# Optimization experiments

Measured on AMD Instinct MI355X. Metric: run time of the kernel, lower is better.

## Reference

```python
import jax, jax.numpy as jnp
import numpy as np

N_NODES = 100000
N_EDGES = 1000000
H = 128


def setup_inputs() -> dict:
    key = jax.random.key(0)
    ks = jax.random.split(key, 8)
    s = 1.0 / np.sqrt(H)
    return {
        "x": jax.random.normal(ks[0], (N_NODES, H), dtype=jnp.float32),
        "edge_index": jax.random.randint(ks[1], (2, N_EDGES), 0, N_NODES, dtype=jnp.int64),
        "W_p": jax.random.normal(ks[2], (H, H), dtype=jnp.float32) * s,
        "b_p": jnp.zeros((H,), dtype=jnp.float32),
        "W_c": jax.random.normal(ks[3], (H, H), dtype=jnp.float32) * s,
        "b_c": jnp.zeros((H,), dtype=jnp.float32),
        "W1": jax.random.normal(ks[4], (3 * H, H), dtype=jnp.float32) * (1.0 / np.sqrt(3 * H)),
        "b1": jnp.zeros((H,), dtype=jnp.float32),
        "W2": jax.random.normal(ks[5], (H, 1), dtype=jnp.float32) * s,
        "b2": jnp.zeros((1,), dtype=jnp.float32),
    }


def reference(x, edge_index, W_p, b_p, W_c, b_c, W1, b1, W2, b2):
    # Gather parent (src) and child (dst) node features per edge: [E, H]
    par_fea = x[edge_index[0]]
    cld_fea = x[edge_index[1]]
    # Dual small MLPs (LeakyReLU slope 0.01, dropout inactive at inference)
    enc_p = jax.nn.leaky_relu(par_fea @ W_p + b_p, negative_slope=0.01)
    enc_c = jax.nn.leaky_relu(cld_fea @ W_c + b_c, negative_slope=0.01)
    diff = jnp.abs(par_fea - cld_fea)
    edge_features = jnp.concatenate([enc_p, enc_c, diff], axis=-1)  # [E, 3H]
    h = jax.nn.relu(edge_features @ W1 + b1)
    edge_weight = jax.nn.sigmoid(h @ W2 + b2).squeeze(-1)  # [E]
    return edge_weight
```

## Files before the change

kernel.cpp:

```cpp
#include <hip/hip_runtime.h>
#include <hip/hip_bf16.h>

#define E_EDGES 1000000
#define N_NODES 100000
#define HDIM 128
#define BM 64
#define LDP 136

typedef __attribute__((ext_vector_type(8))) short short8;
typedef __attribute__((ext_vector_type(4))) float f32x4;

static __device__ __forceinline__ short f2bf(float f) {
  unsigned int u = __float_as_uint(f);
  unsigned int r = (u + 0x7FFFu + ((u >> 16) & 1u)) >> 16;
  return (short)r;
}
static __device__ __forceinline__ float bf2f(short s) {
  return __uint_as_float(((unsigned int)(unsigned short)s) << 16);
}

__global__ void prep_weights(const float* __restrict__ Wp, const float* __restrict__ Wc,
                             const float* __restrict__ W1, const float* __restrict__ W2,
                             short* __restrict__ wp_t, short* __restrict__ wc_t,
                             short* __restrict__ w1_t, float* __restrict__ w2v) {
  int i = blockIdx.x * 256 + threadIdx.x;
  if (i < HDIM * HDIM) {
    int o = i >> 7, k = i & (HDIM - 1);
    wp_t[i] = f2bf(Wp[k * HDIM + o]);
    wc_t[i] = f2bf(Wc[k * HDIM + o]);
  }
  if (i < HDIM * 3 * HDIM) {
    int o = i / (3 * HDIM), k = i - o * (3 * HDIM);
    w1_t[i] = f2bf(W1[k * HDIM + o]);
  }
  if (i < HDIM) w2v[i] = W2[i];
}

__global__ __launch_bounds__(256) void node_precompute(
    const float* __restrict__ x, const float* __restrict__ b_p,
    const float* __restrict__ b_c, const float* __restrict__ b1,
    const short* __restrict__ wp_t, const short* __restrict__ wc_t,
    const short* __restrict__ w1_t,
    short* __restrict__ x_bf, short* __restrict__ Abuf, short* __restrict__ Bbuf) {
  __shared__ __align__(16) short Xt[BM * LDP];
  __shared__ __align__(16) short Yp[BM * LDP];
  __shared__ __align__(16) short Yc[BM * LDP];

  const int t = threadIdx.x;
  const int n0 = blockIdx.x * BM;

  {
    const int lane16 = t & 15, rq = t >> 4, c0 = lane16 * 8;
#pragma unroll
    for (int pass = 0; pass < 4; ++pass) {
      const int row = pass * 16 + rq;
      const int n = n0 + row;
      short8 v;
      if (n < N_NODES) {
        const float* ps = x + (size_t)n * HDIM + c0;
        float4 a = *(const float4*)ps;
        float4 b = *(const float4*)(ps + 4);
        float f[8] = {a.x, a.y, a.z, a.w, b.x, b.y, b.z, b.w};
#pragma unroll
        for (int j = 0; j < 8; ++j) v[j] = f2bf(f[j]);
        *(short8*)&x_bf[(size_t)n * HDIM + c0] = v;
      } else {
#pragma unroll
        for (int j = 0; j < 8; ++j) v[j] = 0;
      }
      *(short8*)&Xt[row * LDP + c0] = v;
    }
  }
  __syncthreads();

  const int l = t & 63;
  const int w = t >> 6;
  const int lr = l & 15;
  const int lg = l >> 4;
  const int aoff = lr * LDP + lg * 8;
  const int na = w * 32 + lr, nb = na + 16;

  const f32x4 zero4 = {0.f, 0.f, 0.f, 0.f};
  f32x4 ap_[4][2], ac_[4][2];
#pragma unroll
  for (int mi = 0; mi < 4; ++mi) {
    ap_[mi][0] = zero4; ap_[mi][1] = zero4;
    ac_[mi][0] = zero4; ac_[mi][1] = zero4;
  }

  const short* wpA = wp_t + na * HDIM + lg * 8;
  const short* wpB = wp_t + nb * HDIM + lg * 8;
  const short* wcA = wc_t + na * HDIM + lg * 8;
  const short* wcB = wc_t + nb * HDIM + lg * 8;

#pragma unroll
  for (int kk = 0; kk < 4; ++kk) {
    short8 b10 = *(const short8*)(wpA + kk * 32);
    short8 b11 = *(const short8*)(wpB + kk * 32);
    short8 b20 = *(const short8*)(wcA + kk * 32);
    short8 b21 = *(const short8*)(wcB + kk * 32);
#pragma unroll
    for (int mi = 0; mi < 4; ++mi) {
      short8 a8 = *(const short8*)&Xt[mi * 16 * LDP + aoff + kk * 32];
      ap_[mi][0] = __builtin_amdgcn_mfma_f32_16x16x32_bf16(a8, b10, ap_[mi][0], 0, 0, 0);
      ap_[mi][1] = __builtin_amdgcn_mfma_f32_16x16x32_bf16(a8, b11, ap_[mi][1], 0, 0, 0);
      ac_[mi][0] = __builtin_amdgcn_mfma_f32_16x16x32_bf16(a8, b20, ac_[mi][0], 0, 0, 0);
      ac_[mi][1] = __builtin_amdgcn_mfma_f32_16x16x32_bf16(a8, b21, ac_[mi][1], 0, 0, 0);
    }
  }

  {
    const float bpa = b_p[na], bpb = b_p[nb];
    const float bca = b_c[na], bcb = b_c[nb];
#pragma unroll
    for (int mi = 0; mi < 4; ++mi) {
#pragma unroll
      for (int r = 0; r < 4; ++r) {
        const int m = mi * 16 + lg * 4 + r;
        float v0 = ap_[mi][0][r] + bpa; v0 = v0 > 0.f ? v0 : 0.01f * v0;
        float v1 = ap_[mi][1][r] + bpb; v1 = v1 > 0.f ? v1 : 0.01f * v1;
        float u0 = ac_[mi][0][r] + bca; u0 = u0 > 0.f ? u0 : 0.01f * u0;
        float u1 = ac_[mi][1][r] + bcb; u1 = u1 > 0.f ? u1 : 0.01f * u1;
        Yp[m * LDP + na] = f2bf(v0);
        Yp[m * LDP + nb] = f2bf(v1);
        Yc[m * LDP + na] = f2bf(u0);
        Yc[m * LDP + nb] = f2bf(u1);
      }
    }
  }
  __syncthreads();

  f32x4 aa_[4][2], ab_[4][2];
#pragma unroll
  for (int mi = 0; mi < 4; ++mi) {
    aa_[mi][0] = zero4; aa_[mi][1] = zero4;
    ab_[mi][0] = zero4; ab_[mi][1] = zero4;
  }
  const short* w1Aa = w1_t + na * (3 * HDIM) + lg * 8;
  const short* w1Ab = w1_t + nb * (3 * HDIM) + lg * 8;
#pragma unroll
  for (int kk = 0; kk < 4; ++kk) {
    short8 ba0 = *(const short8*)(w1Aa + kk * 32);
    short8 ba1 = *(const short8*)(w1Ab + kk * 32);
    short8 bb0 = *(const short8*)(w1Aa + HDIM + kk * 32);
    short8 bb1 = *(const short8*)(w1Ab + HDIM + kk * 32);
#pragma unroll
    for (int mi = 0; mi < 4; ++mi) {
      short8 ayp = *(const short8*)&Yp[mi * 16 * LDP + aoff + kk * 32];
      short8 ayc = *(const short8*)&Yc[mi * 16 * LDP + aoff + kk * 32];
      aa_[mi][0] = __builtin_amdgcn_mfma_f32_16x16x32_bf16(ayp, ba0, aa_[mi][0], 0, 0, 0);
      aa_[mi][1] = __builtin_amdgcn_mfma_f32_16x16x32_bf16(ayp, ba1, aa_[mi][1], 0, 0, 0);
      ab_[mi][0] = __builtin_amdgcn_mfma_f32_16x16x32_bf16(ayc, bb0, ab_[mi][0], 0, 0, 0);
      ab_[mi][1] = __builtin_amdgcn_mfma_f32_16x16x32_bf16(ayc, bb1, ab_[mi][1], 0, 0, 0);
    }
  }

  {
    const float b1a = b1[na], b1b = b1[nb];
#pragma unroll
    for (int mi = 0; mi < 4; ++mi) {
#pragma unroll
      for (int r = 0; r < 4; ++r) {
        const int m = mi * 16 + lg * 4 + r;
        const int n = n0 + m;
        if (n < N_NODES) {
          Abuf[(size_t)n * HDIM + na] = f2bf(aa_[mi][0][r] + b1a);
          Abuf[(size_t)n * HDIM + nb] = f2bf(aa_[mi][1][r] + b1b);
          Bbuf[(size_t)n * HDIM + na] = f2bf(ab_[mi][0][r]);
          Bbuf[(size_t)n * HDIM + nb] = f2bf(ab_[mi][1][r]);
        }
      }
    }
  }
}

__global__ __launch_bounds__(512, 8) void edge_kernel(
    const int* __restrict__ ei, const short* __restrict__ x_bf,
    const short* __restrict__ Abuf, const short* __restrict__ Bbuf,
    const short* __restrict__ w1_t, const float* __restrict__ w2v,
    const float* __restrict__ b2, float* __restrict__ out) {
  __shared__ __align__(16) short Dt[BM * LDP];
  __shared__ float partial[8][BM];

  const int t = threadIdx.x;
  const int e0 = blockIdx.x * BM;

  {
    const int lane16 = t & 15, rq = t >> 4, c0 = lane16 * 8;
#pragma unroll
    for (int pass = 0; pass < 2; ++pass) {
      const int row = pass * 32 + rq;
      const int s = ei[e0 + row];
      const int d = ei[E_EDGES + e0 + row];
      short8 p8 = *(const short8*)(x_bf + (size_t)s * HDIM + c0);
      short8 c8 = *(const short8*)(x_bf + (size_t)d * HDIM + c0);
      short8 v;
#pragma unroll
      for (int j = 0; j < 8; ++j) v[j] = f2bf(fabsf(bf2f(p8[j]) - bf2f(c8[j])));
      *(short8*)&Dt[row * LDP + c0] = v;
    }
  }

  const int l = t & 63;
  const int w = t >> 6;
  const int lr = l & 15;
  const int lg = l >> 4;
  const int na = w * 16 + lr;
  const int aoff = lr * LDP + lg * 8;

  f32x4 acc[4];
#pragma unroll
  for (int mi = 0; mi < 4; ++mi) {
#pragma unroll
    for (int r = 0; r < 4; ++r) {
      const int m = mi * 16 + lg * 4 + r;
      const int s = ei[e0 + m];
      const int d = ei[E_EDGES + e0 + m];
      acc[mi][r] = bf2f(Abuf[(size_t)s * HDIM + na]) + bf2f(Bbuf[(size_t)d * HDIM + na]);
    }
  }
  __syncthreads();

  const short* w1D = w1_t + na * (3 * HDIM) + 2 * HDIM + lg * 8;
#pragma unroll
  for (int kk = 0; kk < 4; ++kk) {
    short8 b8 = *(const short8*)(w1D + kk * 32);
#pragma unroll
    for (int mi = 0; mi < 4; ++mi) {
      short8 a8 = *(const short8*)&Dt[mi * 16 * LDP + aoff + kk * 32];
      acc[mi] = __builtin_amdgcn_mfma_f32_16x16x32_bf16(a8, b8, acc[mi], 0, 0, 0);
    }
  }

  {
    const float w2a = w2v[na];
#pragma unroll
    for (int mi = 0; mi < 4; ++mi) {
#pragma unroll
      for (int r = 0; r < 4; ++r) {
        float h = acc[mi][r] > 0.f ? acc[mi][r] : 0.f;
        float v = h * w2a;
        v += __shfl_xor(v, 1);
        v += __shfl_xor(v, 2);
        v += __shfl_xor(v, 4);
        v += __shfl_xor(v, 8);
        if (lr == 0) partial[w][mi * 16 + lg * 4 + r] = v;
      }
    }
  }
  __syncthreads();

  if (t < BM) {
    float z = partial[0][t] + partial[1][t] + partial[2][t] + partial[3][t] +
              partial[4][t] + partial[5][t] + partial[6][t] + partial[7][t] + b2[0];
    out[e0 + t] = 1.0f / (1.0f + __expf(-z));
  }
}

__global__ __launch_bounds__(512, 4) void edge_weight_fallback(
    const float* __restrict__ x, const int* __restrict__ ei,
    const float* __restrict__ b_p, const float* __restrict__ b_c,
    const float* __restrict__ b1, const float* __restrict__ b2,
    const short* __restrict__ wp_t, const short* __restrict__ wc_t,
    const short* __restrict__ w1_t, const float* __restrict__ w2v,
    float* __restrict__ out) {
  __shared__ __align__(16) short Pt[BM * LDP];
  __shared__ __align__(16) short Ct[BM * LDP];
  __shared__ __align__(16) short Dt[BM * LDP];
  __shared__ float partial[8][BM];

  const int t = threadIdx.x;
  const int e0 = blockIdx.x * BM;
  {
    const int lane16 = t & 15, rq = t >> 4, c0 = lane16 * 8;
#pragma unroll
    for (int pass = 0; pass < 2; ++pass) {
      const int row = pass * 32 + rq;
      const int ip = ei[e0 + row];
      const int ic = ei[E_EDGES + e0 + row];
      const float* ps = x + (size_t)ip * HDIM + c0;
      const float* cs = x + (size_t)ic * HDIM + c0;
      float4 pa = *(const float4*)ps, pb = *(const float4*)(ps + 4);
      float4 ca = *(const float4*)cs, cb = *(const float4*)(cs + 4);
      float pf[8] = {pa.x, pa.y, pa.z, pa.w, pb.x, pb.y, pb.z, pb.w};
      float cf[8] = {ca.x, ca.y, ca.z, ca.w, cb.x, cb.y, cb.z, cb.w};
      short8 vp, vc, vd;
#pragma unroll
      for (int j = 0; j < 8; ++j) {
        vp[j] = f2bf(pf[j]); vc[j] = f2bf(cf[j]); vd[j] = f2bf(fabsf(pf[j] - cf[j]));
      }
      *(short8*)&Pt[row * LDP + c0] = vp;
      *(short8*)&Ct[row * LDP + c0] = vc;
      *(short8*)&Dt[row * LDP + c0] = vd;
    }
  }
  __syncthreads();
  const int l = t & 63, w = t >> 6, lr = l & 15, lg = l >> 4;
  const int n0 = w * 16, na = n0 + lr, aoff = lr * LDP + lg * 8;
  const f32x4 zero4 = {0.f, 0.f, 0.f, 0.f};
  f32x4 acc1[4], acc2[4], acc3[4];
#pragma unroll
  for (int mi = 0; mi < 4; ++mi) { acc1[mi] = zero4; acc2[mi] = zero4; acc3[mi] = zero4; }
  const short* wpA = wp_t + na * HDIM + lg * 8;
  const short* wcA = wc_t + na * HDIM + lg * 8;
  const short* w1A = w1_t + na * (3 * HDIM) + lg * 8;
#pragma unroll
  for (int kk = 0; kk < 4; ++kk) {
    short8 bp8 = *(const short8*)(wpA + kk * 32);
    short8 bc8 = *(const short8*)(wcA + kk * 32);
    short8 bd8 = *(const short8*)(w1A + 2 * HDIM + kk * 32);
#pragma unroll
    for (int mi = 0; mi < 4; ++mi) {
      short8 ap = *(const short8*)&Pt[mi * 16 * LDP + aoff + kk * 32];
      short8 ac = *(const short8*)&Ct[mi * 16 * LDP + aoff + kk * 32];
      short8 ad = *(const short8*)&Dt[mi * 16 * LDP + aoff + kk * 32];
      acc1[mi] = __builtin_amdgcn_mfma_f32_16x16x32_bf16(ap, bp8, acc1[mi], 0, 0, 0);
      acc2[mi] = __builtin_amdgcn_mfma_f32_16x16x32_bf16(ac, bc8, acc2[mi], 0, 0, 0);
      acc3[mi] = __builtin_amdgcn_mfma_f32_16x16x32_bf16(ad, bd8, acc3[mi], 0, 0, 0);
    }
  }
  __syncthreads();
  {
    const float bpa = b_p[na], bca = b_c[na];
#pragma unroll
    for (int mi = 0; mi < 4; ++mi) {
#pragma unroll
      for (int r = 0; r < 4; ++r) {
        const int m = mi * 16 + lg * 4 + r;
        float v0 = acc1[mi][r] + bpa; v0 = v0 > 0.f ? v0 : 0.01f * v0;
        float u0 = acc2[mi][r] + bca; u0 = u0 > 0.f ? u0 : 0.01f * u0;
        Pt[m * LDP + na] = f2bf(v0);
        Ct[m * LDP + na] = f2bf(u0);
      }
    }
  }
  __syncthreads();
#pragma unroll
  for (int kk = 0; kk < 4; ++kk) {
    short8 b0 = *(const short8*)(w1A + kk * 32);
    short8 b1f = *(const short8*)(w1A + HDIM + kk * 32);
#pragma unroll
    for (int mi = 0; mi < 4; ++mi) {
      short8 a0 = *(const short8*)&Pt[mi * 16 * LDP + aoff + kk * 32];
      short8 a1 = *(const short8*)&Ct[mi * 16 * LDP + aoff + kk * 32];
      acc3[mi] = __builtin_amdgcn_mfma_f32_16x16x32_bf16(a0, b0, acc3[mi], 0, 0, 0);
      acc3[mi] = __builtin_amdgcn_mfma_f32_16x16x32_bf16(a1, b1f, acc3[mi], 0, 0, 0);
    }
  }
  {
    const float b1a = b1[na], w2a = w2v[na];
#pragma unroll
    for (int mi = 0; mi < 4; ++mi) {
#pragma unroll
      for (int r = 0; r < 4; ++r) {
        float h0 = acc3[mi][r] + b1a; h0 = h0 > 0.f ? h0 : 0.f;
        float v = h0 * w2a;
        v += __shfl_xor(v, 1); v += __shfl_xor(v, 2);
        v += __shfl_xor(v, 4); v += __shfl_xor(v, 8);
        if (lr == 0) partial[w][mi * 16 + lg * 4 + r] = v;
      }
    }
  }
  __syncthreads();
  if (t < BM) {
    float z = partial[0][t] + partial[1][t] + partial[2][t] + partial[3][t] +
              partial[4][t] + partial[5][t] + partial[6][t] + partial[7][t] + b2[0];
    out[e0 + t] = 1.0f / (1.0f + __expf(-z));
  }
}

extern "C" void kernel_launch(void* const* d_in, const int* in_sizes, int n_in,
                              void* d_out, int out_size, void* d_ws, size_t ws_size,
                              hipStream_t stream) {
  const float* x  = (const float*)d_in[0];
  const int*   ei = (const int*)d_in[1];
  const float* Wp = (const float*)d_in[2];
  const float* bp = (const float*)d_in[3];
  const float* Wc = (const float*)d_in[4];
  const float* bc = (const float*)d_in[5];
  const float* W1 = (const float*)d_in[6];
  const float* b1 = (const float*)d_in[7];
  const float* W2 = (const float*)d_in[8];
  const float* b2 = (const float*)d_in[9];
  float* out = (float*)d_out;

  short* wp_t = (short*)d_ws;
  short* wc_t = wp_t + HDIM * HDIM;
  short* w1_t = wc_t + HDIM * HDIM;
  float* w2v  = (float*)(w1_t + HDIM * 3 * HDIM);
  short* x_bf = (short*)(w2v + HDIM);
  short* Abuf = x_bf + (size_t)N_NODES * HDIM;
  short* Bbuf = Abuf + (size_t)N_NODES * HDIM;

  const size_t needed = (size_t)((char*)(Bbuf + (size_t)N_NODES * HDIM) - (char*)d_ws);

  prep_weights<<<(HDIM * 3 * HDIM + 255) / 256, 256, 0, stream>>>(Wp, Wc, W1, W2,
                                                                  wp_t, wc_t, w1_t, w2v);
  if (ws_size >= needed) {
    node_precompute<<<(N_NODES + BM - 1) / BM, 256, 0, stream>>>(
        x, bp, bc, b1, wp_t, wc_t, w1_t, x_bf, Abuf, Bbuf);
    edge_kernel<<<E_EDGES / BM, 512, 0, stream>>>(ei, x_bf, Abuf, Bbuf, w1_t, w2v, b2, out);
  } else {
    edge_weight_fallback<<<E_EDGES / BM, 512, 0, stream>>>(x, ei, bp, bc, b1, b2,
                                                           wp_t, wc_t, w1_t, w2v, out);
  }
}
```

Before: 221.9 us.

## Coalesce Abuf/Bbuf gathers via vectorized loads staged through shared memory

Replaces per-element scalar gathers of the precomputed Abuf/Bbuf node projections (2-byte loads scattered across rows) with 16-byte vectorized row loads done alongside the x gathers. The summed values are staged in a new float shared-memory tile and read back in the MFMA accumulator layout. Diff conversion also uses a packed bf16x2 round-to-nearest intrinsic. The extra ~33KB of shared memory and the lowered launch-bounds occupancy hint reduce resident blocks per CU.

```diff
diff --git a/kernel.cpp b/kernel.cpp
--- a/kernel.cpp
+++ b/kernel.cpp
@@ -6,6 +6,7 @@
 #define HDIM 128
 #define BM 64
 #define LDP 136
+#define LDS_F 132
 
 typedef __attribute__((ext_vector_type(8))) short short8;
 typedef __attribute__((ext_vector_type(4))) float f32x4;
@@ -17,6 +18,12 @@
 }
 static __device__ __forceinline__ float bf2f(short s) {
   return __uint_as_float(((unsigned int)(unsigned short)s) << 16);
+}
+static __device__ __forceinline__ unsigned int pack_bf16_rn(float lo, float hi) {
+  __hip_bfloat162 h = __float22bfloat162_rn(make_float2(lo, hi));
+  unsigned int u;
+  __builtin_memcpy(&u, &h, 4);
+  return u;
 }
 
 __global__ void prep_weights(const float* __restrict__ Wp, const float* __restrict__ Wc,
@@ -174,12 +181,13 @@
   }
 }
 
-__global__ __launch_bounds__(512, 8) void edge_kernel(
+__global__ __launch_bounds__(512, 4) void edge_kernel(
     const int* __restrict__ ei, const short* __restrict__ x_bf,
     const short* __restrict__ Abuf, const short* __restrict__ Bbuf,
     const short* __restrict__ w1_t, const float* __restrict__ w2v,
     const float* __restrict__ b2, float* __restrict__ out) {
   __shared__ __align__(16) short Dt[BM * LDP];
+  __shared__ __align__(16) float St[BM * LDS_F];
   __shared__ float partial[8][BM];
 
   const int t = threadIdx.x;
@@ -194,12 +202,31 @@
       const int d = ei[E_EDGES + e0 + row];
       short8 p8 = *(const short8*)(x_bf + (size_t)s * HDIM + c0);
       short8 c8 = *(const short8*)(x_bf + (size_t)d * HDIM + c0);
-      short8 v;
-#pragma unroll
-      for (int j = 0; j < 8; ++j) v[j] = f2bf(fabsf(bf2f(p8[j]) - bf2f(c8[j])));
-      *(short8*)&Dt[row * LDP + c0] = v;
-    }
-  }
+      short8 a8 = *(const short8*)(Abuf + (size_t)s * HDIM + c0);
+      short8 b8 = *(const short8*)(Bbuf + (size_t)d * HDIM + c0);
+      float df[8];
+      float4 s0, s1;
+#pragma unroll
+      for (int j = 0; j < 8; ++j) df[j] = fabsf(bf2f(p8[j]) - bf2f(c8[j]));
+      s0.x = bf2f(a8[0]) + bf2f(b8[0]);
+      s0.y = bf2f(a8[1]) + bf2f(b8[1]);
+      s0.z = bf2f(a8[2]) + bf2f(b8[2]);
+      s0.w = bf2f(a8[3]) + bf2f(b8[3]);
+      s1.x = bf2f(a8[4]) + bf2f(b8[4]);
+      s1.y = bf2f(a8[5]) + bf2f(b8[5]);
+      s1.z = bf2f(a8[6]) + bf2f(b8[6]);
+      s1.w = bf2f(a8[7]) + bf2f(b8[7]);
+      uint4 vd;
+      vd.x = pack_bf16_rn(df[0], df[1]);
+      vd.y = pack_bf16_rn(df[2], df[3]);
+      vd.z = pack_bf16_rn(df[4], df[5]);
+      vd.w = pack_bf16_rn(df[6], df[7]);
+      *(uint4*)&Dt[row * LDP + c0] = vd;
+      *(float4*)&St[row * LDS_F + c0] = s0;
+      *(float4*)&St[row * LDS_F + c0 + 4] = s1;
+    }
+  }
+  __syncthreads();
 
   const int l = t & 63;
   const int w = t >> 6;
@@ -213,13 +240,9 @@
   for (int mi = 0; mi < 4; ++mi) {
 #pragma unroll
     for (int r = 0; r < 4; ++r) {
-      const int m = mi * 16 + lg * 4 + r;
-      const int s = ei[e0 + m];
-      const int d = ei[E_EDGES + e0 + m];
-      acc[mi][r] = bf2f(Abuf[(size_t)s * HDIM + na]) + bf2f(Bbuf[(size_t)d * HDIM + na]);
-    }
-  }
-  __syncthreads();
+      acc[mi][r] = St[(mi * 16 + lg * 4 + r) * LDS_F + na];
+    }
+  }
 
   const short* w1D = w1_t + na * (3 * HDIM) + 2 * HDIM + lg * 8;
 #pragma unroll
```

After: 232.0 us. +4.5%, slower.
